# Kernel tuning notes

Measured on AMD Instinct MI355X. Metric: run time of the kernel, lower is better.

Reference implementation:

```python
import jax, jax.numpy as jnp
import numpy as np

B, S, E = 4, 2048, 1024
H, D = 16, 64  # num_heads, attention_head_dim


def setup_inputs() -> dict:
    key = jax.random.key(0)
    ks = jax.random.split(key, 9)
    scale_e = 1.0 / np.sqrt(E)
    scale_hd = 1.0 / np.sqrt(H * D)
    x = jax.random.normal(ks[0], (B, S, E), dtype=jnp.float32)
    # per-head projection weights, stacked: [H, E, D]
    Wq = jax.random.uniform(ks[1], (H, E, D), minval=-scale_e, maxval=scale_e, dtype=jnp.float32)
    Wk = jax.random.uniform(ks[2], (H, E, D), minval=-scale_e, maxval=scale_e, dtype=jnp.float32)
    Wv = jax.random.uniform(ks[3], (H, E, D), minval=-scale_e, maxval=scale_e, dtype=jnp.float32)
    bq = jax.random.uniform(ks[4], (H, D), minval=-scale_e, maxval=scale_e, dtype=jnp.float32)
    bk = jax.random.uniform(ks[5], (H, D), minval=-scale_e, maxval=scale_e, dtype=jnp.float32)
    bv = jax.random.uniform(ks[6], (H, D), minval=-scale_e, maxval=scale_e, dtype=jnp.float32)
    Wo = jax.random.uniform(ks[7], (H * D, E), minval=-scale_hd, maxval=scale_hd, dtype=jnp.float32)
    bo = jax.random.uniform(ks[8], (E,), minval=-scale_hd, maxval=scale_hd, dtype=jnp.float32)
    return {"x": x, "Wq": Wq, "Wk": Wk, "Wv": Wv, "bq": bq, "bk": bk, "bv": bv, "Wo": Wo, "bo": bo}


def reference(x, Wq, Wk, Wv, bq, bk, bv, Wo, bo):
    # Per-head QKV projections, vectorized over heads: [B,H,S,D]
    Q = jnp.einsum('bse,hed->bhsd', x, Wq) + bq[None, :, None, :]
    K = jnp.einsum('bse,hed->bhsd', x, Wk) + bk[None, :, None, :]
    V = jnp.einsum('bse,hed->bhsd', x, Wv) + bv[None, :, None, :]
    scale = 1.0 / jnp.sqrt(jnp.asarray(D, dtype=Q.dtype))
    scores = jnp.einsum('bhsd,bhtd->bhst', Q, K) * scale  # [B,H,S,S]
    attn = jax.nn.softmax(scores, axis=-1)
    Z = jnp.einsum('bhst,bhtd->bhsd', attn, V)            # [B,H,S,D]
    # concat heads on feature dim -> [B,S,H*D], then output projection
    Zc = jnp.transpose(Z, (0, 2, 1, 3)).reshape(B, S, H * D)
    return Zc @ Wo + bo
```

## Files before the change

### kernel.cpp

```cpp
#include <hip/hip_runtime.h>


typedef __attribute__((ext_vector_type(4)))  float   f32x4;
typedef __attribute__((ext_vector_type(16))) float   f32x16;
typedef __attribute__((ext_vector_type(8)))  __bf16  bf16x8;
typedef __attribute__((ext_vector_type(4)))  __bf16  bf16x4;
typedef __attribute__((ext_vector_type(4)))  unsigned int u32x4;
typedef unsigned int u32;

#if __has_builtin(__builtin_amdgcn_exp2f)
#define EXP2F(x) __builtin_amdgcn_exp2f(x)
#else
#define EXP2F(x) exp2f(x)
#endif

__device__ __forceinline__ f32x4 fzero4() {
    f32x4 z = {0.f, 0.f, 0.f, 0.f};
    return z;
}
__device__ __forceinline__ f32x16 fzero16() {
    f32x16 z;
#pragma unroll
    for (int i = 0; i < 16; i++) z[i] = 0.f;
    return z;
}

__device__ __forceinline__ u32 cvtpk_bf16(float lo, float hi_) {
    u32 r;
    asm("v_cvt_pk_bf16_f32 %0, %1, %2" : "=v"(r) : "v"(lo), "v"(hi_));
    return r;
}

__device__ __forceinline__ void gload_lds16(const void* g, void* l) {
    __builtin_amdgcn_global_load_lds(
        (const __attribute__((address_space(1))) u32*)g,
        (__attribute__((address_space(3))) u32*)l, 16, 0, 0);
}

__global__ __launch_bounds__(256) void cvt_f32_bf16_4(
    const float* __restrict__ s, __bf16* __restrict__ d, long n) {
    long i = ((long)blockIdx.x * 256 + threadIdx.x) * 4;
    if (i >= n) return;
    float4 v = *(const float4*)(s + i);
    bf16x4 o = { (__bf16)v.x, (__bf16)v.y, (__bf16)v.z, (__bf16)v.w };
    *(bf16x4*)(d + i) = o;
}

__global__ __launch_bounds__(256) void pack_w_t(
    const float* __restrict__ src, __bf16* __restrict__ dst, int R, int C) {
    __shared__ float t[32][33];
    const int z = blockIdx.z;
    src += (size_t)z * R * C;
    dst += (size_t)z * R * C;
    const int r0 = blockIdx.x * 32, c0 = blockIdx.y * 32;
    const int x = threadIdx.x, y = threadIdx.y;
#pragma unroll
    for (int i = 0; i < 4; i++)
        t[y + i * 8][x] = src[(size_t)(r0 + y + i * 8) * C + c0 + x];
    __syncthreads();
#pragma unroll
    for (int i = 0; i < 4; i++)
        dst[(size_t)(c0 + y + i * 8) * R + r0 + x] = (__bf16)t[x][y + i * 8];
}

__global__ __launch_bounds__(256) void pack_bias(
    const float* __restrict__ bq, const float* __restrict__ bk,
    const float* __restrict__ bv, float* __restrict__ bqkv) {
    int n = blockIdx.x * 256 + threadIdx.x;
    if (n >= 3072) return;
    int t = n >> 10, r = n & 1023;
    const float* s = (t == 0) ? bq : (t == 1) ? bk : bv;
    bqkv[n] = s[r];
}

#define GEMM_STAGE(BUF, KOFF)                                                  \
  {                                                                            \
    gload_lds16(A + arow * K + (KOFF) + kcol,                                  \
                (char*)As + (BUF) * 8192 + wid * 1024);                        \
    gload_lds16(A + (arow + 64) * K + (KOFF) + kcol,                           \
                (char*)As + (BUF) * 8192 + 4096 + wid * 1024);                 \
    gload_lds16(Bt + brow * K + (KOFF) + kcol,                                 \
                (char*)Bs + (BUF) * 8192 + wid * 1024);                        \
    gload_lds16(Bt + (brow + 64) * K + (KOFF) + kcol,                          \
                (char*)Bs + (BUF) * 8192 + 4096 + wid * 1024);                 \
  }

#define GEMM_COMPUTE(BUF)                                                      \
  {                                                                            \
    bf16x8 a[4], b[4];                                                         \
    _Pragma("unroll")                                                          \
    for (int mi = 0; mi < 4; mi++)                                             \
      a[mi] = *(const bf16x8*)&As[(BUF) * 4096 +                               \
                                  (wr * 64 + mi * 16 + l15) * 32 + l4 * 8];    \
    _Pragma("unroll")                                                          \
    for (int ni = 0; ni < 4; ni++)                                             \
      b[ni] = *(const bf16x8*)&Bs[(BUF) * 4096 +                               \
                                  (wc * 64 + ni * 16 + l15) * 32 + l4 * 8];    \
    _Pragma("unroll")                                                          \
    for (int mi = 0; mi < 4; mi++)                                             \
      _Pragma("unroll")                                                        \
      for (int ni = 0; ni < 4; ni++)                                           \
        acc[mi][ni] = __builtin_amdgcn_mfma_f32_16x16x32_bf16(                 \
            a[mi], b[ni], acc[mi][ni], 0, 0, 0);                               \
  }

template <bool F32OUT>
__global__ __launch_bounds__(256) void gemm_bt(
    const __bf16* __restrict__ A, const __bf16* __restrict__ Bt,
    const float* __restrict__ bias, void* __restrict__ Cout,
    int M, int N, int K, int ldc) {
    __shared__ __bf16 As[2 * 128 * 32];
    __shared__ __bf16 Bs[2 * 128 * 32];
    const int tid  = threadIdx.x;
    const int lane = tid & 63, wid = tid >> 6;
    const int wr = wid >> 1, wc = wid & 1;
    const int l15 = lane & 15, l4 = lane >> 4;
    const int bn = blockIdx.x, bm = blockIdx.y;
    const long arow = (long)bm * 128 + (tid >> 2);
    const long brow = (long)bn * 128 + (tid >> 2);
    const int  kcol = (tid & 3) * 8;

    f32x4 acc[4][4];
#pragma unroll
    for (int i = 0; i < 4; i++)
#pragma unroll
        for (int j = 0; j < 4; j++) acc[i][j] = fzero4();

    GEMM_STAGE(0, 0)
    __syncthreads();
    int cur = 0;
    for (int k0 = 0; k0 < K; k0 += 32, cur ^= 1) {
        if (k0 + 32 < K) GEMM_STAGE(cur ^ 1, k0 + 32)
        GEMM_COMPUTE(cur)
        __syncthreads();
    }

#pragma unroll
    for (int mi = 0; mi < 4; mi++)
#pragma unroll
        for (int ni = 0; ni < 4; ni++) {
            const int row = bm * 128 + wr * 64 + mi * 16 + l4 * 4;
            const int col = bn * 128 + wc * 64 + ni * 16 + l15;
            const float bv = bias ? bias[col] : 0.f;
#pragma unroll
            for (int r = 0; r < 4; r++) {
                float v = acc[mi][ni][r] + bv;
                if (F32OUT)
                    ((float*)Cout)[(long)(row + r) * ldc + col] = v;
                else
                    ((__bf16*)Cout)[(long)(row + r) * ldc + col] = (__bf16)v;
            }
        }
}

__global__ __launch_bounds__(256) void gemm_qkv(
    const __bf16* __restrict__ A, const __bf16* __restrict__ Bt,
    const float* __restrict__ bias, __bf16* __restrict__ QKV,
    __bf16* __restrict__ VT, int K) {
    __shared__ __bf16 As[2 * 128 * 32];
    __shared__ __bf16 Bs[2 * 128 * 32];
    const int tid  = threadIdx.x;
    const int lane = tid & 63, wid = tid >> 6;
    const int wr = wid >> 1, wc = wid & 1;
    const int l15 = lane & 15, l4 = lane >> 4;
    const int bn = blockIdx.x, bm = blockIdx.y;
    const long arow = (long)bm * 128 + (tid >> 2);
    const long brow = (long)bn * 128 + (tid >> 2);
    const int  kcol = (tid & 3) * 8;

    f32x4 acc[4][4];
#pragma unroll
    for (int i = 0; i < 4; i++)
#pragma unroll
        for (int j = 0; j < 4; j++) acc[i][j] = fzero4();

    GEMM_STAGE(0, 0)
    __syncthreads();
    int cur = 0;
    for (int k0 = 0; k0 < K; k0 += 32, cur ^= 1) {
        if (k0 + 32 < K) GEMM_STAGE(cur ^ 1, k0 + 32)
        GEMM_COMPUTE(cur)
        __syncthreads();
    }

    if (bn < 16) {
#pragma unroll
        for (int mi = 0; mi < 4; mi++)
#pragma unroll
            for (int ni = 0; ni < 4; ni++) {
                const int row = bm * 128 + wr * 64 + mi * 16 + l4 * 4;
                const int col = bn * 128 + wc * 64 + ni * 16 + l15;
                const float bv = bias[col];
#pragma unroll
                for (int r = 0; r < 4; r++)
                    QKV[(long)(row + r) * 3072 + col] =
                        (__bf16)(acc[mi][ni][r] + bv);
            }
    } else {
#pragma unroll
        for (int mi = 0; mi < 4; mi++)
#pragma unroll
            for (int ni = 0; ni < 4; ni++) {
                const int row = bm * 128 + wr * 64 + mi * 16 + l4 * 4;
                const int col = bn * 128 + wc * 64 + ni * 16 + l15;
                const float bv = bias[col];
                const int vcol = col - 2048;
                const int h = vcol >> 6, dcol = vcol & 63;
                const int bb = row >> 11, s = row & 2047;
                bf16x4 o;
#pragma unroll
                for (int r = 0; r < 4; r++)
                    o[r] = (__bf16)(acc[mi][ni][r] + bv);
                *(bf16x4*)&VT[((size_t)(bb * 16 + h) * 64 + dcol) * 2048 + s] = o;
            }
    }
}

__global__ __launch_bounds__(256, 4) void attn_fwd(
    const __bf16* __restrict__ QKV, const __bf16* __restrict__ VT,
    __bf16* __restrict__ Z) {
    const int S = 2048, LDQ = 3072;
    const int dd = blockIdx.x;
    const int blk = (dd & 7) * 128 + (dd >> 3);
    const int qt = blk & 15, bh = blk >> 4, b = bh >> 4, h = bh & 15;
    const int tid = threadIdx.x, wid = tid >> 6, lane = tid & 63;
    const int l31 = lane & 31, hi = lane >> 5;

    __shared__ __bf16 smem[16384];

    const __bf16* Qb = QKV + (size_t)b * S * LDQ + h * 64;
    const __bf16* Kb = Qb + 1024;
    const __bf16* Vb = VT + (size_t)bh * 64 * S;
    const int qrow = qt * 128 + wid * 32;

    bf16x8 qf[4];
#pragma unroll
    for (int kk = 0; kk < 4; kk++)
        qf[kk] = *(const bf16x8*)(Qb + (size_t)(qrow + l31) * LDQ + kk * 16 + hi * 8);

    const int f0 = wid * 2, f1 = wid * 2 + 1;
    const int kr0 = (f0 >> 2) * 32 + l31, kc0 = (f0 & 3) * 16 + hi * 8;
    const int kr1 = (f1 >> 2) * 32 + l31, kc1 = (f1 & 3) * 16 + hi * 8;
    const int vr0 = kr0, vs0 = kc0;
    const int vr1 = kr1, vs1 = kc1;
    const int ldst = lane * 16;

    f32x16 o0 = fzero16(), o1 = fzero16();
    float m_r = -1e30f, l_r = 0.f;
    const float csc = 0.18033688011f;

    gload_lds16(Kb + (size_t)kr0 * LDQ + kc0, (char*)smem + f0 * 1024 + ldst);
    gload_lds16(Kb + (size_t)kr1 * LDQ + kc1, (char*)smem + f1 * 1024 + ldst);
    gload_lds16(Vb + (size_t)vr0 * S + vs0,   (char*)smem + 16384 + f0 * 1024 + ldst);
    gload_lds16(Vb + (size_t)vr1 * S + vs1,   (char*)smem + 16384 + f1 * 1024 + ldst);
    asm volatile("s_waitcnt vmcnt(0)" ::: "memory");
    __syncthreads();

    int cur = 0;
    for (int t0 = 0; t0 < S; t0 += 64, cur ^= 1) {
        if (t0 + 64 < S) {
            char* kl = (char*)smem + (cur ^ 1) * 8192;
            char* vl = (char*)smem + 16384 + (cur ^ 1) * 8192;
            gload_lds16(Kb + (size_t)(t0 + 64 + kr0) * LDQ + kc0, kl + f0 * 1024 + ldst);
            gload_lds16(Kb + (size_t)(t0 + 64 + kr1) * LDQ + kc1, kl + f1 * 1024 + ldst);
            gload_lds16(Vb + (size_t)vr0 * S + t0 + 64 + vs0,     vl + f0 * 1024 + ldst);
            gload_lds16(Vb + (size_t)vr1 * S + t0 + 64 + vs1,     vl + f1 * 1024 + ldst);
        }
        const char* kbase = (const char*)smem + cur * 8192;
        const char* vbase = (const char*)smem + 16384 + cur * 8192;

        bf16x8 kf[8];
#pragma unroll
        for (int f = 0; f < 8; f++)
            kf[f] = *(const bf16x8*)(kbase + f * 1024 + ldst);
        f32x16 s0 = fzero16(), s1 = fzero16();
        __builtin_amdgcn_s_setprio(1);
#pragma unroll
        for (int kk = 0; kk < 4; kk++) {
            s0 = __builtin_amdgcn_mfma_f32_32x32x16_bf16(kf[kk],     qf[kk], s0, 0, 0, 0);
            s1 = __builtin_amdgcn_mfma_f32_32x32x16_bf16(kf[4 + kk], qf[kk], s1, 0, 0, 0);
        }
        __builtin_amdgcn_s_setprio(0);

        float mm[16];
#pragma unroll
        for (int i = 0; i < 16; i++) mm[i] = fmaxf(s0[i], s1[i]);
#pragma unroll
        for (int st = 8; st >= 1; st >>= 1)
#pragma unroll
            for (int i = 0; i < st; i++) mm[i] = fmaxf(mm[i], mm[i + st]);
        const float pm = fmaxf(mm[0], __shfl_xor(mm[0], 32));
        if (!__all(pm - m_r <= 64.f)) {
            const float mnew = fmaxf(m_r, pm);
            const float alpha = EXP2F((m_r - mnew) * csc);
            m_r = mnew;
            l_r *= alpha;
#pragma unroll
            for (int i = 0; i < 16; i++) { o0[i] *= alpha; o1[i] *= alpha; }
        }
        const float mc = m_r * csc;
        float ss[16];
#pragma unroll
        for (int i = 0; i < 16; i++) {
            float p0 = EXP2F(s0[i] * csc - mc); s0[i] = p0;
            float p1 = EXP2F(s1[i] * csc - mc); s1[i] = p1;
            ss[i] = p0 + p1;
        }
#pragma unroll
        for (int st = 8; st >= 1; st >>= 1)
#pragma unroll
            for (int i = 0; i < st; i++) ss[i] += ss[i + st];
        l_r += ss[0] + __shfl_xor(ss[0], 32);

        __builtin_amdgcn_s_setprio(1);
#pragma unroll
        for (int kkt = 0; kkt < 4; kkt++) {
            const int r0 = (kkt & 1) * 8;
            u32 w0, w1, w2, w3;
            if (kkt < 2) {
                w0 = cvtpk_bf16(s0[r0],     s0[r0 + 1]);
                w1 = cvtpk_bf16(s0[r0 + 2], s0[r0 + 3]);
                w2 = cvtpk_bf16(s0[r0 + 4], s0[r0 + 5]);
                w3 = cvtpk_bf16(s0[r0 + 6], s0[r0 + 7]);
            } else {
                w0 = cvtpk_bf16(s1[r0],     s1[r0 + 1]);
                w1 = cvtpk_bf16(s1[r0 + 2], s1[r0 + 3]);
                w2 = cvtpk_bf16(s1[r0 + 4], s1[r0 + 5]);
                w3 = cvtpk_bf16(s1[r0 + 6], s1[r0 + 7]);
            }
            asm("v_permlane32_swap_b32 %0, %1" : "+v"(w0), "+v"(w2));
            asm("v_permlane32_swap_b32 %0, %1" : "+v"(w1), "+v"(w3));
            u32x4 pw = {w0, w1, w2, w3};
            bf16x8 pf = __builtin_bit_cast(bf16x8, pw);
            bf16x8 vf0 = *(const bf16x8*)(vbase + kkt * 1024 + ldst);
            bf16x8 vf1 = *(const bf16x8*)(vbase + (4 + kkt) * 1024 + ldst);
            o0 = __builtin_amdgcn_mfma_f32_32x32x16_bf16(vf0, pf, o0, 0, 0, 0);
            o1 = __builtin_amdgcn_mfma_f32_32x32x16_bf16(vf1, pf, o1, 0, 0, 0);
        }
        __builtin_amdgcn_s_setprio(0);

        asm volatile("s_waitcnt vmcnt(0)" ::: "memory");
        __syncthreads();
    }

    const float inv = 1.0f / l_r;
    __bf16 (*Tl)[72] = (__bf16 (*)[72])smem;
    const int trow = wid * 32 + l31;
#pragma unroll
    for (int g = 0; g < 4; g++) {
        bf16x4 t4a, t4b;
#pragma unroll
        for (int j = 0; j < 4; j++) {
            t4a[j] = (__bf16)(o0[4 * g + j] * inv);
            t4b[j] = (__bf16)(o1[4 * g + j] * inv);
        }
        *(bf16x4*)&Tl[trow][g * 8 + hi * 4]      = t4a;
        *(bf16x4*)&Tl[trow][32 + g * 8 + hi * 4] = t4b;
    }
    asm volatile("s_waitcnt lgkmcnt(0)" ::: "memory");
    __builtin_amdgcn_sched_barrier(0);

    const int rr = wid * 32 + (lane >> 1);
    const int ch = (lane & 1) * 32;
#pragma unroll
    for (int i = 0; i < 4; i++) {
        bf16x8 z = *(const bf16x8*)&Tl[rr][ch + i * 8];
        *(bf16x8*)&Z[((size_t)b * S + qt * 128 + rr) * 1024 + h * 64 + ch + i * 8] = z;
    }
}

extern "C" void kernel_launch(void* const* d_in, const int* in_sizes, int n_in,
                              void* d_out, int out_size, void* d_ws, size_t ws_size,
                              hipStream_t stream) {
    const float* x  = (const float*)d_in[0];
    const float* Wq = (const float*)d_in[1];
    const float* Wk = (const float*)d_in[2];
    const float* Wv = (const float*)d_in[3];
    const float* bq = (const float*)d_in[4];
    const float* bk = (const float*)d_in[5];
    const float* bv = (const float*)d_in[6];
    const float* Wo = (const float*)d_in[7];
    const float* bo = (const float*)d_in[8];
    float* out = (float*)d_out;

    char* p = (char*)d_ws;
    __bf16* xb   = (__bf16*)p; p += 8192L * 1024 * 2;
    __bf16* Wqkv = (__bf16*)p; p += 3072L * 1024 * 2;
    float*  bqkv = (float*)p;  p += 3072L * 4;
    __bf16* QKV  = (__bf16*)p; p += 8192L * 3072 * 2;
    __bf16* VTb  = (__bf16*)p; p += 64L * 64 * 2048 * 2;
    __bf16* Zb   = (__bf16*)p; p += 8192L * 1024 * 2;
    __bf16* Wot  = (__bf16*)p; p += 1024L * 1024 * 2;

    cvt_f32_bf16_4<<<8192, 256, 0, stream>>>(x, xb, 8192L * 1024);
    pack_w_t<<<dim3(32, 2, 16), dim3(32, 8), 0, stream>>>(Wq, Wqkv,                1024, 64);
    pack_w_t<<<dim3(32, 2, 16), dim3(32, 8), 0, stream>>>(Wk, Wqkv + 1024L * 1024, 1024, 64);
    pack_w_t<<<dim3(32, 2, 16), dim3(32, 8), 0, stream>>>(Wv, Wqkv + 2048L * 1024, 1024, 64);
    pack_w_t<<<dim3(32, 32, 1), dim3(32, 8), 0, stream>>>(Wo, Wot, 1024, 1024);
    pack_bias<<<12, 256, 0, stream>>>(bq, bk, bv, bqkv);

    gemm_qkv<<<dim3(24, 64), 256, 0, stream>>>(xb, Wqkv, bqkv, QKV, VTb, 1024);
    attn_fwd<<<1024, 256, 0, stream>>>(QKV, VTb, Zb);
    gemm_bt<true><<<dim3(8, 64), 256, 0, stream>>>(Zb, Wot, bo, out,
                                                   8192, 1024, 1024, 1024);
}
```

Before: 226.8 us.

## Triple-buffer GEMM shared-memory tiles with explicit waitcnt and single barrier

Both the generic GEMM and the fused QKV-projection GEMM move from a double-buffered K loop to a three-stage ring of shared-memory tiles. Two stages are prefetched up front. Each iteration waits only on the oldest outstanding global loads (`vmcnt(4)`), then issues one barrier before launching the load two tiles ahead. This is meant to hide more global-memory latency and remove the second `__syncthreads` per iteration. In exchange, shared memory per block grows by half, which can reduce occupancy. The hand-written waitcnt counts also rely on the exact number of loads each stage issues.

```diff
diff --git a/kernel.cpp b/kernel.cpp
--- a/kernel.cpp
+++ b/kernel.cpp
@@ -104,13 +104,33 @@
             a[mi], b[ni], acc[mi][ni], 0, 0, 0);                               \
   }
 
+#define GEMM_PIPE_LOOP                                                         \
+  GEMM_STAGE(0, 0)                                                             \
+  GEMM_STAGE(1, 32)                                                            \
+  int kt = 0;                                                                  \
+  for (int k0 = 0; k0 < K; k0 += 32, kt++) {                                   \
+    asm volatile("s_waitcnt lgkmcnt(0)" ::: "memory");                         \
+    if (k0 + 32 < K) {                                                         \
+      asm volatile("s_waitcnt vmcnt(4)" ::: "memory");                         \
+    } else {                                                                   \
+      asm volatile("s_waitcnt vmcnt(0)" ::: "memory");                         \
+    }                                                                          \
+    __builtin_amdgcn_s_barrier();                                              \
+    if (k0 + 64 < K) {                                                         \
+      const int nb = (kt + 2) % 3;                                             \
+      GEMM_STAGE(nb, k0 + 64)                                                  \
+    }                                                                          \
+    const int cb = kt % 3;                                                     \
+    GEMM_COMPUTE(cb)                                                           \
+  }
+
 template <bool F32OUT>
 __global__ __launch_bounds__(256) void gemm_bt(
     const __bf16* __restrict__ A, const __bf16* __restrict__ Bt,
     const float* __restrict__ bias, void* __restrict__ Cout,
     int M, int N, int K, int ldc) {
-    __shared__ __bf16 As[2 * 128 * 32];
-    __shared__ __bf16 Bs[2 * 128 * 32];
+    __shared__ __bf16 As[3 * 128 * 32];
+    __shared__ __bf16 Bs[3 * 128 * 32];
     const int tid  = threadIdx.x;
     const int lane = tid & 63, wid = tid >> 6;
     const int wr = wid >> 1, wc = wid & 1;
@@ -126,14 +146,7 @@
 #pragma unroll
         for (int j = 0; j < 4; j++) acc[i][j] = fzero4();
 
-    GEMM_STAGE(0, 0)
-    __syncthreads();
-    int cur = 0;
-    for (int k0 = 0; k0 < K; k0 += 32, cur ^= 1) {
-        if (k0 + 32 < K) GEMM_STAGE(cur ^ 1, k0 + 32)
-        GEMM_COMPUTE(cur)
-        __syncthreads();
-    }
+    GEMM_PIPE_LOOP
 
 #pragma unroll
     for (int mi = 0; mi < 4; mi++)
@@ -157,8 +170,8 @@
     const __bf16* __restrict__ A, const __bf16* __restrict__ Bt,
     const float* __restrict__ bias, __bf16* __restrict__ QKV,
     __bf16* __restrict__ VT, int K) {
-    __shared__ __bf16 As[2 * 128 * 32];
-    __shared__ __bf16 Bs[2 * 128 * 32];
+    __shared__ __bf16 As[3 * 128 * 32];
+    __shared__ __bf16 Bs[3 * 128 * 32];
     const int tid  = threadIdx.x;
     const int lane = tid & 63, wid = tid >> 6;
     const int wr = wid >> 1, wc = wid & 1;
@@ -174,14 +187,7 @@
 #pragma unroll
         for (int j = 0; j < 4; j++) acc[i][j] = fzero4();
 
-    GEMM_STAGE(0, 0)
-    __syncthreads();
-    int cur = 0;
-    for (int k0 = 0; k0 < K; k0 += 32, cur ^= 1) {
-        if (k0 + 32 < K) GEMM_STAGE(cur ^ 1, k0 + 32)
-        GEMM_COMPUTE(cur)
-        __syncthreads();
-    }
+    GEMM_PIPE_LOOP
 
     if (bn < 16) {
 #pragma unroll
```

Result: no change. 228.8 us (+0.9%).
